# Optimization experiments

Hardware: AMD Instinct MI355X
Metric: run time of the kernel (lower is better)

## Reference

```python
import jax, jax.numpy as jnp
import numpy as np

VOCAB, EMBED, HIDDEN = 32000, 512, 1024
B, T = 8, 256

def setup_inputs() -> dict:
    key = jax.random.key(0)
    ks = jax.random.split(key, 5)
    x = jax.random.randint(ks[0], (B, T), 0, VOCAB)
    embedding = jax.random.normal(ks[1], (VOCAB, EMBED), dtype=jnp.float32)
    W_xh = jax.random.normal(ks[2], (EMBED, HIDDEN), dtype=jnp.float32) * 0.01
    W_hh = jax.random.normal(ks[3], (HIDDEN, HIDDEN), dtype=jnp.float32) * 0.01
    b_h = jnp.zeros((HIDDEN,), dtype=jnp.float32)
    W_hy = jax.random.normal(ks[4], (HIDDEN, VOCAB), dtype=jnp.float32) * 0.01
    b_y = jnp.zeros((VOCAB,), dtype=jnp.float32)
    return {"x": x, "embedding": embedding, "W_xh": W_xh, "W_hh": W_hh,
            "b_h": b_h, "W_hy": W_hy, "b_y": b_y}

def reference(x, embedding, W_xh, W_hh, b_h, W_hy, b_y):
    # x: [B,T] int ids
    emb = embedding[x]                      # [B,T,E]
    # Precompute input contribution for all steps: [B,T,H]
    xh = jnp.einsum('bte,eh->bth', emb, W_xh) + b_h
    h0 = jnp.zeros((x.shape[0], W_hh.shape[0]), dtype=emb.dtype)

    def step(h, xh_t):
        h = jnp.tanh(xh_t + h @ W_hh)       # [B,H]
        return h, h

    _, hs = jax.lax.scan(step, h0, jnp.swapaxes(xh, 0, 1))  # hs: [T,B,H]
    hs = jnp.swapaxes(hs, 0, 1)             # [B,T,H]
    # Output projection batched over all timesteps (same math as per-step)
    y = jnp.einsum('bth,hv->btv', hs, W_hy) + b_y  # [B,T,V]
    return y
```

## Files before the change

kernel.cpp:

```cpp
#include <hip/hip_runtime.h>
#include <hip/hip_bf16.h>

#define VOCAB 32000
#define EMBED 512
#define HIDDEN 1024
#define NB 8
#define NT 256
#define XH_ROWS 16

#define NCH 8
#define NMEM 32
#define RCOLS 32
#define NBLK_REC 256
#define NBLK_TR 128
#define TILES_PER_TR 250

typedef __attribute__((ext_vector_type(8))) short bf16x8;
typedef __attribute__((ext_vector_type(4))) float f32x4;
typedef __attribute__((ext_vector_type(4))) unsigned u32x4;

#define AS1 __attribute__((address_space(1)))
#define AS3 __attribute__((address_space(3)))

__device__ __forceinline__ unsigned short bf16_bits(float f) {
    __hip_bfloat16 b = __float2bfloat16(f);
    unsigned short s;
    __builtin_memcpy(&s, &b, 2);
    return s;
}
__device__ __forceinline__ float lo16f(unsigned u) { return __uint_as_float(u << 16); }
__device__ __forceinline__ float hi16f(unsigned u) { return __uint_as_float(u & 0xffff0000u); }

__global__ __launch_bounds__(256) void k_xh(const int* __restrict__ ids,
                                            const float* __restrict__ emb,
                                            const float* __restrict__ Wxh,
                                            const float* __restrict__ bh,
                                            float* __restrict__ xh) {
    __shared__ alignas(16) float embS[XH_ROWS][EMBED];
    __shared__ int idsS[XH_ROWS];
    const int tid = threadIdx.x;
    const int blk = blockIdx.x;
    if (tid < XH_ROWS) idsS[tid] = ids[blk * XH_ROWS + tid];
    __syncthreads();
    const float4* emb4 = (const float4*)emb;
#pragma unroll
    for (int rep = 0; rep < (XH_ROWS * EMBED / 4) / 256; ++rep) {
        const int lin = rep * 256 + tid;
        const int r = lin >> 7;
        const int e4 = lin & 127;
        *(float4*)&embS[r][e4 * 4] = emb4[(size_t)idsS[r] * (EMBED / 4) + e4];
    }
    __syncthreads();
    float4 acc[XH_ROWS] = {};
    const float4* W4 = (const float4*)Wxh;
    for (int e = 0; e < EMBED; ++e) {
        const float4 w = W4[(size_t)e * (HIDDEN / 4) + tid];
#pragma unroll
        for (int r = 0; r < XH_ROWS; ++r) {
            const float ev = embS[r][e];
            acc[r].x += ev * w.x; acc[r].y += ev * w.y;
            acc[r].z += ev * w.z; acc[r].w += ev * w.w;
        }
    }
    const float4 bv = ((const float4*)bh)[tid];
#pragma unroll
    for (int r = 0; r < XH_ROWS; ++r) {
        float4 o;
        o.x = acc[r].x + bv.x; o.y = acc[r].y + bv.y;
        o.z = acc[r].z + bv.z; o.w = acc[r].w + bv.w;
        ((float4*)xh)[(size_t)(blk * XH_ROWS + r) * (HIDDEN / 4) + tid] = o;
    }
}

__global__ __launch_bounds__(256, 1) void k_fused(const float* __restrict__ Whh,
                                                  const float* __restrict__ xh,
                                                  unsigned long long* __restrict__ hx,
                                                  __hip_bfloat16* __restrict__ hs,
                                                  const float* __restrict__ Why,
                                                  __hip_bfloat16* __restrict__ Wt) {
    __shared__ alignas(16) float smemF[9808];
    float* xhS = smemF;
    float* hS  = smemF + 8192;
    float* red = smemF + 9280;
    const int tid = threadIdx.x;
    const int bid = blockIdx.x;

    if (bid >= NBLK_REC) {
        const int tb = bid - NBLK_REC;
        const int cc = tid & 31;
        const int r0 = tid >> 5;
        const int tbase = tb * TILES_PER_TR;
        for (int rnd = 0; rnd < (TILES_PER_TR + 7) / 8; ++rnd) {
            const int base = rnd * 8;
            __syncthreads();
#pragma unroll
            for (int u = 0; u < 8; ++u) {
                const int i = base + u;
                if (i < TILES_PER_TR) {
                    const int g = tbase + i;
                    const int n0 = (g % 1000) * 32;
                    const int k0 = (g / 1000) * 32;
                    float* tile = smemF + u * 1056;
#pragma unroll
                    for (int rr = 0; rr < 4; ++rr) {
                        const int r = r0 + rr * 8;
                        tile[cc * 33 + r] = Why[(size_t)(k0 + r) * VOCAB + n0 + cc];
                    }
                }
            }
            __syncthreads();
#pragma unroll
            for (int u = 0; u < 8; ++u) {
                const int i = base + u;
                if (i < TILES_PER_TR) {
                    const int g = tbase + i;
                    const int n0 = (g % 1000) * 32;
                    const int k0 = (g / 1000) * 32;
                    float* tile = smemF + u * 1056;
#pragma unroll
                    for (int rr = 0; rr < 4; ++rr) {
                        const int n = r0 + rr * 8;
                        Wt[(size_t)(n0 + n) * HIDDEN + k0 + cc] = __float2bfloat16(tile[n * 33 + cc]);
                    }
                }
            }
        }
        return;
    }

    const int c = bid & (NCH - 1);
    const int m = bid >> 3;
    const int j0 = m * RCOLS;
    unsigned long long* hxc = hx + (size_t)c * 1024;

    if (tid < 16)
        __hip_atomic_store(&hxc[512 + m * 16 + tid], 0ull, __ATOMIC_RELAXED,
                           __HIP_MEMORY_SCOPE_AGENT);

    const int col2 = tid & 15;
    const int part = tid >> 4;

    u32x4 wreg[16];
#pragma unroll
    for (int j = 0; j < 16; ++j) {
        u32x4 q;
#pragma unroll
        for (int e = 0; e < 4; ++e) {
            const int i = part * 64 + 4 * j + e;
            const float2 wv = *(const float2*)&Whh[(size_t)i * HIDDEN + j0 + 2 * col2];
            q[e] = (unsigned)bf16_bits(wv.x) | ((unsigned)bf16_bits(wv.y) << 16);
        }
        wreg[j] = q;
    }
    for (int idx = tid; idx < NT * RCOLS; idx += 256) {
        const int t = idx >> 5;
        const int col = idx & 31;
        xhS[idx] = xh[(size_t)(c * NT + t) * HIDDEN + j0 + col];
    }
    __syncthreads();

    const f32x4* hv4 = (const f32x4*)&hS[part * 68];
    const int w0 = tid;
    const int w1 = tid + 256;
    const int pe0 = 2 * tid + 4 * (tid >> 5);

    for (int t = 0; t < NT; ++t) {
        unsigned long long* rbuf = hxc + ((t + 1) & 1) * 512;
        unsigned long long* wbuf = hxc + (t & 1) * 512;
        const unsigned long long tok = (unsigned long long)(unsigned)t;
        unsigned long long a = __hip_atomic_load(&rbuf[w0], __ATOMIC_RELAXED, __HIP_MEMORY_SCOPE_AGENT);
        unsigned long long b = __hip_atomic_load(&rbuf[w1], __ATOMIC_RELAXED, __HIP_MEMORY_SCOPE_AGENT);
        while (((a & 0xffffull) != tok) | ((b & 0xffffull) != tok)) {
            __builtin_amdgcn_s_sleep(1);
            if ((a & 0xffffull) != tok)
                a = __hip_atomic_load(&rbuf[w0], __ATOMIC_RELAXED, __HIP_MEMORY_SCOPE_AGENT);
            if ((b & 0xffffull) != tok)
                b = __hip_atomic_load(&rbuf[w1], __ATOMIC_RELAXED, __HIP_MEMORY_SCOPE_AGENT);
        }
        *(float2*)&hS[pe0] = make_float2(__uint_as_float(((unsigned)(a >> 16) & 0xffffu) << 16),
                                         __uint_as_float(((unsigned)(a >> 32) & 0xffffu) << 16));
        *(float2*)&hS[pe0 + 544] = make_float2(__uint_as_float(((unsigned)(b >> 16) & 0xffffu) << 16),
                                               __uint_as_float(((unsigned)(b >> 32) & 0xffffu) << 16));
        __syncthreads();
        float a0 = 0.f, a1 = 0.f;
#pragma unroll
        for (int j = 0; j < 16; ++j) {
            const u32x4 w4 = wreg[j];
            const f32x4 h4 = hv4[j];
            a0 = fmaf(lo16f(w4.x), h4.x, a0); a1 = fmaf(hi16f(w4.x), h4.x, a1);
            a0 = fmaf(lo16f(w4.y), h4.y, a0); a1 = fmaf(hi16f(w4.y), h4.y, a1);
            a0 = fmaf(lo16f(w4.z), h4.z, a0); a1 = fmaf(hi16f(w4.z), h4.z, a1);
            a0 = fmaf(lo16f(w4.w), h4.w, a0); a1 = fmaf(hi16f(w4.w), h4.w, a1);
        }
        red[part * 33 + 2 * col2]     = a0;
        red[part * 33 + 2 * col2 + 1] = a1;
        __syncthreads();
        if (tid < RCOLS) {
            float s = 0.f;
#pragma unroll
            for (int p = 0; p < 16; ++p) s += red[p * 33 + tid];
            const float v = tanhf(xhS[t * RCOLS + tid] + s);
            const unsigned hb = (unsigned)bf16_bits(v);
            ((unsigned short*)hs)[(size_t)(c * NT + t) * HIDDEN + j0 + tid] = (unsigned short)hb;
            const unsigned pb = (unsigned)__shfl_xor((int)hb, 1, 64);
            if ((tid & 1) == 0) {
                const unsigned long long wv = (unsigned long long)(unsigned)(t + 1)
                                            | ((unsigned long long)hb << 16)
                                            | ((unsigned long long)pb << 32);
                __hip_atomic_store(&wbuf[m * 16 + (tid >> 1)], wv, __ATOMIC_RELAXED,
                                   __HIP_MEMORY_SCOPE_AGENT);
            }
        }
    }
}

__global__ __launch_bounds__(512, 2) void k_proj(const unsigned short* __restrict__ A,
                                                 const unsigned short* __restrict__ Bt,
                                                 const float* __restrict__ by,
                                                 float* __restrict__ C) {
    __shared__ unsigned short LDS[2][2][8192];
    const int tid = threadIdx.x;
    const int wid = tid >> 6;
    const int lane = tid & 63;
    const int lin = blockIdx.x;
    const int swz = (lin & 7) * 125 + (lin >> 3);
    const int mt = swz & 7, nt = swz >> 3;
    const int m0 = mt * 256, n0 = nt * 256;
    const int wr = wid >> 2, wc = wid & 3;
    const int fr = lane & 15, fq = lane >> 4;

    f32x4 acc[8][4] = {};

#define STAGE(kt, bf)                                                                     \
    {                                                                                     \
        const unsigned short* Ag = A + (size_t)m0 * HIDDEN + (size_t)(kt) * 32;           \
        const unsigned short* Bg = Bt + (size_t)n0 * HIDDEN + (size_t)(kt) * 32;          \
        _Pragma("unroll")                                                                 \
        for (int s2 = 0; s2 < 2; ++s2) {                                                  \
            const int ch = s2 * 512 + tid;                                                \
            const int row = ch >> 2, sp = ch & 3;                                         \
            const int gs = sp ^ ((row >> 1) & 3);                                         \
            __builtin_amdgcn_global_load_lds(                                             \
                (const AS1 unsigned*)(Ag + (size_t)row * HIDDEN + gs * 8),                \
                (AS3 unsigned*)(&LDS[bf][0][(s2 * 512 + wid * 64) * 8]), 16, 0, 0);       \
        }                                                                                 \
        _Pragma("unroll")                                                                 \
        for (int s2 = 0; s2 < 2; ++s2) {                                                  \
            const int ch = s2 * 512 + tid;                                                \
            const int row = ch >> 2, sp = ch & 3;                                         \
            const int gs = sp ^ ((row >> 1) & 3);                                         \
            __builtin_amdgcn_global_load_lds(                                             \
                (const AS1 unsigned*)(Bg + (size_t)row * HIDDEN + gs * 8),                \
                (AS3 unsigned*)(&LDS[bf][1][(s2 * 512 + wid * 64) * 8]), 16, 0, 0);       \
        }                                                                                 \
    }

    STAGE(0, 0);
    STAGE(1, 1);

    int cur = 0;
    for (int kt = 0; kt < 32; ++kt) {
        if (kt < 31) { asm volatile("s_waitcnt vmcnt(4)" ::: "memory"); }
        else         { asm volatile("s_waitcnt vmcnt(0)" ::: "memory"); }
        __builtin_amdgcn_s_barrier();

        const unsigned short* Ab = &LDS[cur][0][0];
        const unsigned short* Bb = &LDS[cur][1][0];
        bf16x8 af[8], bg[4];
#pragma unroll
        for (int mi = 0; mi < 8; ++mi) {
            const int ra = wr * 128 + mi * 16 + fr;
            af[mi] = *(const bf16x8*)&Ab[ra * 32 + ((fq ^ ((ra >> 1) & 3)) * 8)];
        }
#pragma unroll
        for (int ni = 0; ni < 4; ++ni) {
            const int rb = wc * 64 + ni * 16 + fr;
            bg[ni] = *(const bf16x8*)&Bb[rb * 32 + ((fq ^ ((rb >> 1) & 3)) * 8)];
        }
        asm volatile("s_waitcnt lgkmcnt(0)" ::: "memory");
        __builtin_amdgcn_sched_barrier(0);
        __builtin_amdgcn_s_barrier();

        if (kt < 30) STAGE(kt + 2, cur);

        __builtin_amdgcn_s_setprio(1);
#pragma unroll
        for (int mi = 0; mi < 8; ++mi)
#pragma unroll
            for (int ni = 0; ni < 4; ++ni)
                acc[mi][ni] = __builtin_amdgcn_mfma_f32_16x16x32_bf16(af[mi], bg[ni], acc[mi][ni], 0, 0, 0);
        __builtin_amdgcn_s_setprio(0);
        cur ^= 1;
    }
#undef STAGE

#pragma unroll
    for (int ni = 0; ni < 4; ++ni) {
        const int col = n0 + wc * 64 + ni * 16 + fr;
        const float bias = by[col];
#pragma unroll
        for (int mi = 0; mi < 8; ++mi) {
            const int row = m0 + wr * 128 + mi * 16 + fq * 4;
            float* cp = C + (size_t)row * VOCAB + col;
            cp[0]                 = acc[mi][ni][0] + bias;
            cp[(size_t)VOCAB]     = acc[mi][ni][1] + bias;
            cp[(size_t)2 * VOCAB] = acc[mi][ni][2] + bias;
            cp[(size_t)3 * VOCAB] = acc[mi][ni][3] + bias;
        }
    }
}

extern "C" void kernel_launch(void* const* d_in, const int* in_sizes, int n_in,
                              void* d_out, int out_size, void* d_ws, size_t ws_size,
                              hipStream_t stream) {
    const int*   x   = (const int*)d_in[0];
    const float* emb = (const float*)d_in[1];
    const float* Wxh = (const float*)d_in[2];
    const float* Whh = (const float*)d_in[3];
    const float* bh  = (const float*)d_in[4];
    const float* Why = (const float*)d_in[5];
    const float* by  = (const float*)d_in[6];
    float* y = (float*)d_out;

    char* ws = (char*)d_ws;
    const size_t off_xh = 0;
    const size_t off_hx = off_xh + (size_t)NB * NT * HIDDEN * 4;
    const size_t off_hs = off_hx + (size_t)NCH * 2 * 512 * 8;
    const size_t off_wt = off_hs + (size_t)NB * NT * HIDDEN * 2;
    const size_t need   = off_wt + (size_t)VOCAB * HIDDEN * 2;
    if (ws_size < need) return;

    float* xh = (float*)(ws + off_xh);
    unsigned long long* hx = (unsigned long long*)(ws + off_hx);
    __hip_bfloat16* hs = (__hip_bfloat16*)(ws + off_hs);
    __hip_bfloat16* Wt = (__hip_bfloat16*)(ws + off_wt);

    k_xh<<<dim3((NB * NT) / XH_ROWS), 256, 0, stream>>>(x, emb, Wxh, bh, xh);
    k_fused<<<dim3(NBLK_REC + NBLK_TR), 256, 0, stream>>>(Whh, xh, hx, hs, Why, Wt);
    k_proj<<<dim3((2048 / 256) * (VOCAB / 256)), 512, 0, stream>>>((const unsigned short*)hs,
                                                                   (const unsigned short*)Wt, by, y);
}
```

Measured before the change: 798.0 us.

## Restructure projection GEMM into 8-phase half-tile pipeline with K=64 tiles

The output projection GEMM moves from K=32 double-buffered tiles to K=64 tiles split into half-tiles, with loads, LDS reads and MFMA quarters interleaved across eight barrier-separated phases per iteration. The LDS layout changes to 64-wide rows with an 8-way XOR swizzle, and LDS use grows to 128KB. The goal is to overlap global-to-LDS staging with matrix math at finer granularity and to issue fewer waits per K step. In exchange the higher LDS footprint likely limits occupancy to one block per CU despite launch_bounds(512,2), and many barriers are added.

```diff
diff --git a/kernel.cpp b/kernel.cpp
--- a/kernel.cpp
+++ b/kernel.cpp
@@ -218,7 +218,7 @@
                                                  const unsigned short* __restrict__ Bt,
                                                  const float* __restrict__ by,
                                                  float* __restrict__ C) {
-    __shared__ unsigned short LDS[2][2][8192];
+    __shared__ unsigned short LDSu[8 * 8192];
     const int tid = threadIdx.x;
     const int wid = tid >> 6;
     const int lane = tid & 63;
@@ -230,69 +230,113 @@
     const int fr = lane & 15, fq = lane >> 4;
 
     f32x4 acc[8][4] = {};
-
-#define STAGE(kt, bf)                                                                     \
-    {                                                                                     \
-        const unsigned short* Ag = A + (size_t)m0 * HIDDEN + (size_t)(kt) * 32;           \
-        const unsigned short* Bg = Bt + (size_t)n0 * HIDDEN + (size_t)(kt) * 32;          \
+    bf16x8 af[2][4][2];
+    bf16x8 bg[2][2][2];
+
+#define VMC0   asm volatile("s_waitcnt vmcnt(0)" ::: "memory")
+#define LGKM0  do { asm volatile("s_waitcnt lgkmcnt(0)" ::: "memory"); \
+                    __builtin_amdgcn_sched_barrier(0); } while (0)
+#define BAR    __builtin_amdgcn_s_barrier()
+
+#define STAGE_HALF(SRC, ROW0, KT, B_, MAT, H)                                             \
+    do {                                                                                  \
+        const unsigned short* g_ = (SRC) + (size_t)((ROW0) + (H) * 128) * HIDDEN + (KT) * 64; \
         _Pragma("unroll")                                                                 \
         for (int s2 = 0; s2 < 2; ++s2) {                                                  \
-            const int ch = s2 * 512 + tid;                                                \
-            const int row = ch >> 2, sp = ch & 3;                                         \
-            const int gs = sp ^ ((row >> 1) & 3);                                         \
+            const int ch_ = s2 * 512 + tid;                                               \
+            const int lr_ = ch_ >> 3, sp_ = ch_ & 7;                                      \
+            const int gs_ = sp_ ^ (lr_ & 7);                                              \
             __builtin_amdgcn_global_load_lds(                                             \
-                (const AS1 unsigned*)(Ag + (size_t)row * HIDDEN + gs * 8),                \
-                (AS3 unsigned*)(&LDS[bf][0][(s2 * 512 + wid * 64) * 8]), 16, 0, 0);       \
+                (const AS1 unsigned*)(g_ + (size_t)lr_ * HIDDEN + gs_ * 8),               \
+                (AS3 unsigned*)(LDSu + ((B_) * 4 + (MAT) * 2 + (H)) * 8192                \
+                                + (s2 * 512 + wid * 64) * 8), 16, 0, 0);                  \
         }                                                                                 \
+    } while (0)
+
+#define READ_AF(B_, MH)                                                                   \
+    do {                                                                                  \
+        const unsigned short* r_ = LDSu + ((B_) * 4 + wr) * 8192;                         \
         _Pragma("unroll")                                                                 \
-        for (int s2 = 0; s2 < 2; ++s2) {                                                  \
-            const int ch = s2 * 512 + tid;                                                \
-            const int row = ch >> 2, sp = ch & 3;                                         \
-            const int gs = sp ^ ((row >> 1) & 3);                                         \
-            __builtin_amdgcn_global_load_lds(                                             \
-                (const AS1 unsigned*)(Bg + (size_t)row * HIDDEN + gs * 8),                \
-                (AS3 unsigned*)(&LDS[bf][1][(s2 * 512 + wid * 64) * 8]), 16, 0, 0);       \
+        for (int q_ = 0; q_ < 4; ++q_) {                                                  \
+            const int lr_ = ((MH) * 4 + q_) * 16 + fr;                                    \
+            _Pragma("unroll")                                                             \
+            for (int ks_ = 0; ks_ < 2; ++ks_)                                             \
+                af[MH][q_][ks_] = *(const bf16x8*)&r_[lr_ * 64 + (((ks_ * 4 + fq) ^ (fr & 7)) * 8)]; \
         }                                                                                 \
-    }
-
-    STAGE(0, 0);
-    STAGE(1, 1);
-
-    int cur = 0;
-    for (int kt = 0; kt < 32; ++kt) {
-        if (kt < 31) { asm volatile("s_waitcnt vmcnt(4)" ::: "memory"); }
-        else         { asm volatile("s_waitcnt vmcnt(0)" ::: "memory"); }
-        __builtin_amdgcn_s_barrier();
-
-        const unsigned short* Ab = &LDS[cur][0][0];
-        const unsigned short* Bb = &LDS[cur][1][0];
-        bf16x8 af[8], bg[4];
-#pragma unroll
-        for (int mi = 0; mi < 8; ++mi) {
-            const int ra = wr * 128 + mi * 16 + fr;
-            af[mi] = *(const bf16x8*)&Ab[ra * 32 + ((fq ^ ((ra >> 1) & 3)) * 8)];
-        }
-#pragma unroll
-        for (int ni = 0; ni < 4; ++ni) {
-            const int rb = wc * 64 + ni * 16 + fr;
-            bg[ni] = *(const bf16x8*)&Bb[rb * 32 + ((fq ^ ((rb >> 1) & 3)) * 8)];
-        }
-        asm volatile("s_waitcnt lgkmcnt(0)" ::: "memory");
-        __builtin_amdgcn_sched_barrier(0);
-        __builtin_amdgcn_s_barrier();
-
-        if (kt < 30) STAGE(kt + 2, cur);
-
-        __builtin_amdgcn_s_setprio(1);
-#pragma unroll
-        for (int mi = 0; mi < 8; ++mi)
-#pragma unroll
-            for (int ni = 0; ni < 4; ++ni)
-                acc[mi][ni] = __builtin_amdgcn_mfma_f32_16x16x32_bf16(af[mi], bg[ni], acc[mi][ni], 0, 0, 0);
-        __builtin_amdgcn_s_setprio(0);
-        cur ^= 1;
-    }
-#undef STAGE
+    } while (0)
+
+#define READ_BG(B_, NH)                                                                   \
+    do {                                                                                  \
+        const unsigned short* r_ = LDSu + ((B_) * 4 + 2 + (wc >> 1)) * 8192;              \
+        _Pragma("unroll")                                                                 \
+        for (int j_ = 0; j_ < 2; ++j_) {                                                  \
+            const int lr_ = (wc & 1) * 64 + ((NH) * 2 + j_) * 16 + fr;                    \
+            _Pragma("unroll")                                                             \
+            for (int ks_ = 0; ks_ < 2; ++ks_)                                             \
+                bg[NH][j_][ks_] = *(const bf16x8*)&r_[lr_ * 64 + (((ks_ * 4 + fq) ^ (fr & 7)) * 8)]; \
+        }                                                                                 \
+    } while (0)
+
+#define MFMA16(MH, NH)                                                                    \
+    do {                                                                                  \
+        __builtin_amdgcn_s_setprio(1);                                                    \
+        _Pragma("unroll")                                                                 \
+        for (int q_ = 0; q_ < 4; ++q_)                                                    \
+            _Pragma("unroll")                                                             \
+            for (int j_ = 0; j_ < 2; ++j_) {                                              \
+                acc[(MH) * 4 + q_][(NH) * 2 + j_] = __builtin_amdgcn_mfma_f32_16x16x32_bf16( \
+                    af[MH][q_][0], bg[NH][j_][0], acc[(MH) * 4 + q_][(NH) * 2 + j_], 0, 0, 0); \
+                acc[(MH) * 4 + q_][(NH) * 2 + j_] = __builtin_amdgcn_mfma_f32_16x16x32_bf16( \
+                    af[MH][q_][1], bg[NH][j_][1], acc[(MH) * 4 + q_][(NH) * 2 + j_], 0, 0, 0); \
+            }                                                                             \
+        __builtin_amdgcn_s_setprio(0);                                                    \
+    } while (0)
+
+    STAGE_HALF(Bt, n0, 0, 0, 1, 0);
+    STAGE_HALF(Bt, n0, 0, 0, 1, 1);
+    STAGE_HALF(A,  m0, 0, 0, 0, 0);
+    STAGE_HALF(A,  m0, 0, 0, 0, 1);
+    STAGE_HALF(Bt, n0, 1, 1, 1, 0);
+    VMC0;
+    BAR;
+
+    for (int i = 0; i < 8; ++i) {
+        const int t_b1cur = 2 * i + 1;
+        const int t_b0nxt = 2 * i + 2;
+        const int t_b1nxt = 2 * i + 3;
+        READ_AF(0, 0); READ_BG(0, 0);
+        STAGE_HALF(Bt, n0, t_b1cur, 1, 1, 1);
+        BAR; LGKM0; MFMA16(0, 0); BAR;
+        READ_BG(0, 1);
+        STAGE_HALF(A, m0, t_b1cur, 1, 0, 0);
+        BAR; LGKM0; MFMA16(0, 1); BAR;
+        READ_AF(0, 1);
+        STAGE_HALF(A, m0, t_b1cur, 1, 0, 1);
+        BAR; LGKM0; MFMA16(1, 0); BAR;
+        VMC0;
+        if (t_b0nxt < 16) STAGE_HALF(Bt, n0, t_b0nxt, 0, 1, 0);
+        BAR; MFMA16(1, 1); BAR;
+        READ_AF(1, 0); READ_BG(1, 0);
+        if (t_b0nxt < 16) STAGE_HALF(Bt, n0, t_b0nxt, 0, 1, 1);
+        BAR; LGKM0; MFMA16(0, 0); BAR;
+        READ_BG(1, 1);
+        if (t_b0nxt < 16) STAGE_HALF(A, m0, t_b0nxt, 0, 0, 0);
+        BAR; LGKM0; MFMA16(0, 1); BAR;
+        READ_AF(1, 1);
+        if (t_b0nxt < 16) STAGE_HALF(A, m0, t_b0nxt, 0, 0, 1);
+        BAR; LGKM0; MFMA16(1, 0); BAR;
+        VMC0;
+        if (t_b1nxt < 16) STAGE_HALF(Bt, n0, t_b1nxt, 1, 1, 0);
+        BAR; MFMA16(1, 1); BAR;
+    }
+
+#undef VMC0
+#undef LGKM0
+#undef BAR
+#undef STAGE_HALF
+#undef READ_AF
+#undef READ_BG
+#undef MFMA16
 
 #pragma unroll
     for (int ni = 0; ni < 4; ++ni) {
```

New measurement: 792.9 us (median of 2 runs). Within noise of the previous version (-0.6%).
